# Performance work log

Hardware: AMD Instinct MI355X
Metric: run time of the kernel (lower is better)

The kernel has to match this reference:

```python
import jax, jax.numpy as jnp
import numpy as np

EPS = 1e-5

def setup_inputs() -> dict:
    key = jax.random.key(0)
    ks = jax.random.split(key, 8)
    B, T, D, S = 8, 4096, 1024, 64
    return {
        "x": jax.random.normal(ks[0], (B, T, D), dtype=jnp.float32),
        "time_decay": jax.random.normal(ks[1], (S,), dtype=jnp.float32) * 0.1 - 0.5,
        "time_first": jax.random.normal(ks[2], (S,), dtype=jnp.float32) * 0.1,
        "W_key": jax.random.normal(ks[3], (S, D), dtype=jnp.float32) * 0.02,
        "W_value": jax.random.normal(ks[4], (S, D), dtype=jnp.float32) * 0.02,
        "W_output": jax.random.normal(ks[5], (D, S), dtype=jnp.float32) * 0.02,
        "W_shift": jax.random.normal(ks[6], (D, D), dtype=jnp.float32) * 0.02,
        "shift_gate": jnp.ones((D,), dtype=jnp.float32),
        "ln_w": jnp.ones((D,), dtype=jnp.float32),
        "ln_b": jnp.zeros((D,), dtype=jnp.float32),
    }


def _forward(x, time_decay, time_first, W_key, W_value, W_output, W_shift, shift_gate, ln_w, ln_b):
    B, T, D = x.shape
    S = time_decay.shape[0]
    # --- token shift: rotate sequence by shift_len, project, gated blend ---
    shift_len = max(1, int(T * 0.5))
    x_cat = jnp.concatenate([x[:, shift_len:], x[:, :-shift_len]], axis=1)  # (B,T,D)
    gate = jax.nn.sigmoid(shift_gate)
    x_shift = jnp.einsum('btd,ed->bte', x_cat, W_shift) * gate + x * (1.0 - gate)
    # --- layernorm (torch: biased variance, eps=1e-5) ---
    mu = jnp.mean(x_shift, axis=-1, keepdims=True)
    var = jnp.mean(jnp.square(x_shift - mu), axis=-1, keepdims=True)
    xn = (x_shift - mu) * jax.lax.rsqrt(var + EPS) * ln_w + ln_b
    # --- key/value projections and per-step wkv (fully vectorized) ---
    k = jnp.einsum('btd,sd->bts', xn, W_key)    # (B,T,S)
    v = jnp.einsum('btd,sd->bts', xn, W_value)  # (B,T,S)
    wkv = jnp.exp(-jnp.exp(time_first) * jax.nn.sigmoid(k)) * v  # (B,T,S)
    # --- linear recurrence: state = state*w + wkv_t, scanned over T ---
    w = jnp.exp(time_decay)  # (S,)
    def step(state, wkv_t):
        state = state * w + wkv_t
        return state, state
    init = jnp.zeros((B, S), dtype=x.dtype)
    last_state, states = jax.lax.scan(step, init, jnp.swapaxes(wkv, 0, 1))  # states: (T,B,S)
    states = jnp.swapaxes(states, 0, 1)  # (B,T,S)
    # --- batched output projection (applied per-step in torch; same math) ---
    output = jnp.einsum('bts,ds->btd', states, W_output)  # (B,T,D)
    return output, last_state


def reference(x, time_decay, time_first, W_key, W_value, W_output, W_shift, shift_gate, ln_w, ln_b):
    out, last_state = _forward(x, time_decay, time_first, W_key, W_value, W_output, W_shift, shift_gate, ln_w, ln_b)
    return out, jax.lax.stop_gradient(last_state)
```

## Files before the change

kernel.cpp:

```cpp
#include <hip/hip_runtime.h>
#include <stdint.h>

#define B_ 8
#define T_ 4096
#define D_ 1024
#define S_ 64
#define N_ 32768
#define OUT_ELEMS 33554432
#define NCHK 128
#define CHKL 32

typedef __attribute__((ext_vector_type(8))) short bf16x8;
typedef __attribute__((ext_vector_type(8))) unsigned short u16x8;
typedef __attribute__((ext_vector_type(4))) float f32x4;

__device__ __forceinline__ uint16_t f2bf(float f) {
    union { float f; uint32_t u; } v; v.f = f;
    uint32_t r = v.u + 0x7FFFu + ((v.u >> 16) & 1u);
    return (uint16_t)(r >> 16);
}
__device__ __forceinline__ float bf2f(uint16_t h) {
    union { uint32_t u; float f; } v; v.u = ((uint32_t)h) << 16;
    return v.f;
}

#define GLOAD_LDS16(gp, lp)                                             \
    __builtin_amdgcn_global_load_lds(                                   \
        (const __attribute__((address_space(1))) void*)(gp),            \
        (__attribute__((address_space(3))) void*)(lp), 16, 0, 0)

__global__ void prep(const float* __restrict__ x,
                     const float* __restrict__ Wsf, const float* __restrict__ Wkf,
                     const float* __restrict__ Wvf, const float* __restrict__ Wof,
                     const float* __restrict__ sg, const float* __restrict__ tf,
                     const float* __restrict__ lnw, const float* __restrict__ lnb,
                     uint16_t* __restrict__ xb, uint16_t* __restrict__ Wsb,
                     uint16_t* __restrict__ Wkvb, uint16_t* __restrict__ Wob,
                     float* __restrict__ gbuf, float* __restrict__ efirst,
                     float* __restrict__ ucvec)
{
    __shared__ float red[4];
    const int blk = blockIdx.x, tid = threadIdx.x;
    if (blk < 2048) {
        for (int i = blk * 256 + tid; i < OUT_ELEMS / 4; i += 2048 * 256) {
            float4 v = ((const float4*)x)[i];
            ushort4 o;
            o.x = f2bf(v.x); o.y = f2bf(v.y); o.z = f2bf(v.z); o.w = f2bf(v.w);
            ((ushort4*)xb)[i] = o;
        }
        return;
    }
    if (blk < 3298) {
        int i = (blk - 2048) * 256 + tid;
        const float* src; uint16_t* dst; int j; bool fold = false;
        if (i < 262144) { src = Wsf; dst = Wsb; j = i; }
        else if (i < 278528) { src = Wkf; dst = Wkvb; j = i - 262144; fold = true; }
        else if (i < 294912) { src = Wvf; dst = Wkvb + 65536; j = i - 278528; fold = true; }
        else if (i < 311296) { src = Wof; dst = Wob; j = i - 294912; }
        else if (i < 311552) {
            j = i - 311296;
            float4 v = ((const float4*)sg)[j];
            float4 g;
            g.x = 1.f / (1.f + __expf(-v.x)); g.y = 1.f / (1.f + __expf(-v.y));
            g.z = 1.f / (1.f + __expf(-v.z)); g.w = 1.f / (1.f + __expf(-v.w));
            ((float4*)gbuf)[j] = g;
            return;
        } else if (i < 311568) {
            j = i - 311552;
            float4 v = ((const float4*)tf)[j];
            float4 e;
            e.x = __expf(v.x); e.y = __expf(v.y); e.z = __expf(v.z); e.w = __expf(v.w);
            ((float4*)efirst)[j] = e;
            return;
        } else return;
        float4 v = ((const float4*)src)[j];
        if (fold) {
            float4 l = ((const float4*)lnw)[j & 255];
            v.x *= l.x; v.y *= l.y; v.z *= l.z; v.w *= l.w;
        }
        ushort4 o;
        o.x = f2bf(v.x); o.y = f2bf(v.y); o.z = f2bf(v.z); o.w = f2bf(v.w);
        ((ushort4*)dst)[j] = o;
        return;
    }
    {
        int b2 = blk - 3298;
        int which = b2 >> 6, s = b2 & 63;
        const float* W = (which < 2) ? Wkf : Wvf;
        const float* L = (which & 1) ? lnb : lnw;
        float4 wv = ((const float4*)W)[s * 256 + tid];
        float4 lv = ((const float4*)L)[tid];
        float p = wv.x * lv.x + wv.y * lv.y + wv.z * lv.z + wv.w * lv.w;
#pragma unroll
        for (int off = 32; off; off >>= 1) p += __shfl_xor(p, off);
        if ((tid & 63) == 0) red[tid >> 6] = p;
        __syncthreads();
        if (tid == 0) ucvec[which * 64 + s] = red[0] + red[1] + red[2] + red[3];
    }
}

__global__ __launch_bounds__(256) void k1_shift_gemm(
    const uint16_t* __restrict__ xb, const uint16_t* __restrict__ Wsb,
    const float* __restrict__ gbuf, uint16_t* __restrict__ xs)
{
    __shared__ char sh[34816];
    uint16_t (*As)[64] = (uint16_t(*)[64])sh;
    uint16_t (*Bs)[64] = (uint16_t(*)[64])(sh + 16384);
    float (*epi)[68] = (float(*)[68])sh;

    const int tid = threadIdx.x;
    const int w = tid >> 6, lane = tid & 63, quad = lane >> 4, l16 = lane & 15;
    const int wm = w >> 1, wn = w & 1;
    const int lin = blockIdx.x;
    const int mt = (lin & 7) * 32 + (lin >> 6);
    const int nt = (lin >> 3) & 7;
    const int m0 = mt * 128, n0 = nt * 128;
    const int m0x = m0 ^ 2048;

    const int srow = w * 32 + (lane >> 3);
    const int scg  = ((lane & 7) ^ ((lane >> 3) & 7)) * 8;
    const uint16_t* aG = xb  + (size_t)(m0x + srow) * D_ + scg;
    const uint16_t* bG = Wsb + (size_t)(n0  + srow) * D_ + scg;

    f32x4 acc[4][4];
#pragma unroll
    for (int i = 0; i < 4; ++i)
#pragma unroll
        for (int j = 0; j < 4; ++j) acc[i][j] = (f32x4){0.f, 0.f, 0.f, 0.f};

    for (int k0 = 0; k0 < D_; k0 += 64) {
        __syncthreads();
#pragma unroll
        for (int i = 0; i < 4; ++i) {
            GLOAD_LDS16(aG + k0 + (size_t)(i * 8) * D_, &As[w * 32 + i * 8][0]);
            GLOAD_LDS16(bG + k0 + (size_t)(i * 8) * D_, &Bs[w * 32 + i * 8][0]);
        }
        __syncthreads();
#pragma unroll
        for (int ks = 0; ks < 2; ++ks) {
            bf16x8 a[4], b[4];
#pragma unroll
            for (int i = 0; i < 4; ++i)
                a[i] = *(const bf16x8*)&As[wm * 64 + i * 16 + l16]
                                         [(((ks * 4 + quad) ^ (l16 & 7)) * 8)];
#pragma unroll
            for (int j = 0; j < 4; ++j)
                b[j] = *(const bf16x8*)&Bs[wn * 64 + j * 16 + l16]
                                         [(((ks * 4 + quad) ^ (l16 & 7)) * 8)];
#pragma unroll
            for (int i = 0; i < 4; ++i)
#pragma unroll
                for (int j = 0; j < 4; ++j)
                    acc[i][j] = __builtin_amdgcn_mfma_f32_16x16x32_bf16(
                        a[i], b[j], acc[i][j], 0, 0, 0);
        }
    }

    const int row = tid >> 1;
    const int c0 = (tid & 1) * 32;
#pragma unroll
    for (int h = 0; h < 2; ++h) {
        __syncthreads();
        if (wn == h) {
#pragma unroll
            for (int i = 0; i < 4; ++i)
#pragma unroll
                for (int j = 0; j < 4; ++j)
#pragma unroll
                    for (int r = 0; r < 4; ++r)
                        epi[wm * 64 + i * 16 + quad * 4 + r][j * 16 + l16] =
                            acc[i][j][r];
        }
        __syncthreads();
        const int col = n0 + h * 64 + c0;
        const uint16_t* xrow = xb + (size_t)(m0 + row) * D_ + col;
        uint16_t* orow = xs + (size_t)(m0 + row) * D_ + col;
#pragma unroll
        for (int c4 = 0; c4 < 8; ++c4) {
            float4 g4 = ((const float4*)(gbuf + col))[c4];
            ushort4 xh = ((const ushort4*)xrow)[c4];
            const float* e = &epi[row][c0 + c4 * 4];
            ushort4 o;
            o.x = f2bf(e[0] * g4.x + bf2f(xh.x) * (1.f - g4.x));
            o.y = f2bf(e[1] * g4.y + bf2f(xh.y) * (1.f - g4.y));
            o.z = f2bf(e[2] * g4.z + bf2f(xh.z) * (1.f - g4.z));
            o.w = f2bf(e[3] * g4.w + bf2f(xh.w) * (1.f - g4.w));
            ((ushort4*)orow)[c4] = o;
        }
    }
}

__global__ __launch_bounds__(256) void k3_kv(
    const uint16_t* __restrict__ xsb, const uint16_t* __restrict__ Wkvb,
    const float* __restrict__ efirst, const float* __restrict__ ucvec,
    float* __restrict__ wkv)
{
    __shared__ char sh[34816];
    uint16_t (*As)[64] = (uint16_t(*)[64])sh;
    uint16_t (*Bs)[64] = (uint16_t(*)[64])(sh + 8192);
    float (*epi)[132] = (float(*)[132])sh;
    float* ssh = (float*)(sh + 33792);
    float* qsh = (float*)(sh + 34048);

    const int tid = threadIdx.x;
    const int w = tid >> 6, lane = tid & 63, quad = lane >> 4, l16 = lane & 15;
    const int wm = w >> 1, wn = w & 1;
    const int m0 = blockIdx.x * 64;

    const int lrow = w * 8 + (lane >> 3);
    const int scg  = ((lane & 7) ^ ((lane >> 3) & 7)) * 8;
    const uint16_t* aG = xsb + (size_t)(m0 + lrow) * D_ + scg;
    const uint16_t* bG = Wkvb + (size_t)lrow * D_ + scg;

    f32x4 acc[2][4];
#pragma unroll
    for (int i = 0; i < 2; ++i)
#pragma unroll
        for (int j = 0; j < 4; ++j) acc[i][j] = (f32x4){0.f, 0.f, 0.f, 0.f};
    f32x4 accs[2], accq[2];
#pragma unroll
    for (int i = 0; i < 2; ++i) {
        accs[i] = (f32x4){0.f, 0.f, 0.f, 0.f};
        accq[i] = (f32x4){0.f, 0.f, 0.f, 0.f};
    }
    bf16x8 ones;
#pragma unroll
    for (int j = 0; j < 8; ++j) ones[j] = (short)0x3F80;

    for (int k0 = 0; k0 < D_; k0 += 64) {
        __syncthreads();
#pragma unroll
        for (int i = 0; i < 2; ++i)
            GLOAD_LDS16(aG + k0 + (size_t)(i * 32) * D_, &As[w * 8 + i * 32][0]);
#pragma unroll
        for (int i = 0; i < 4; ++i)
            GLOAD_LDS16(bG + k0 + (size_t)(i * 32) * D_, &Bs[w * 8 + i * 32][0]);
        __syncthreads();
#pragma unroll
        for (int ks = 0; ks < 2; ++ks) {
            bf16x8 a[2], b[4];
#pragma unroll
            for (int i = 0; i < 2; ++i)
                a[i] = *(const bf16x8*)&As[wm * 32 + i * 16 + l16]
                                         [(((ks * 4 + quad) ^ (l16 & 7)) * 8)];
#pragma unroll
            for (int j = 0; j < 4; ++j)
                b[j] = *(const bf16x8*)&Bs[wn * 64 + j * 16 + l16]
                                         [(((ks * 4 + quad) ^ (l16 & 7)) * 8)];
#pragma unroll
            for (int i = 0; i < 2; ++i)
#pragma unroll
                for (int j = 0; j < 4; ++j)
                    acc[i][j] = __builtin_amdgcn_mfma_f32_16x16x32_bf16(
                        a[i], b[j], acc[i][j], 0, 0, 0);
            if (wn == 0) {
#pragma unroll
                for (int i = 0; i < 2; ++i) {
                    accs[i] = __builtin_amdgcn_mfma_f32_16x16x32_bf16(
                        a[i], ones, accs[i], 0, 0, 0);
                    accq[i] = __builtin_amdgcn_mfma_f32_16x16x32_bf16(
                        a[i], a[i], accq[i], 0, 0, 0);
                }
            }
        }
    }

    if (wn == 0) {
#pragma unroll
        for (int i = 0; i < 2; ++i) {
            if (l16 == 0) {
#pragma unroll
                for (int r = 0; r < 4; ++r)
                    ssh[wm * 32 + i * 16 + quad * 4 + r] = accs[i][r];
            }
            if ((l16 >> 2) == quad)
                qsh[wm * 32 + i * 16 + l16] = accq[i][l16 & 3];
        }
    }

    __syncthreads();
#pragma unroll
    for (int i = 0; i < 2; ++i)
#pragma unroll
        for (int j = 0; j < 4; ++j)
#pragma unroll
            for (int r = 0; r < 4; ++r)
                epi[wm * 32 + i * 16 + quad * 4 + r][wn * 64 + j * 16 + l16] =
                    acc[i][j][r];
    __syncthreads();

    const int row = tid >> 2, s0 = (tid & 3) * 16;
    const float mu = ssh[row] * (1.f / (float)D_);
    const float var = qsh[row] * (1.f / (float)D_) - mu * mu;
    const float rstd = rsqrtf(var + 1e-5f);
    float* dst = wkv + (size_t)(m0 + row) * S_ + s0;
#pragma unroll
    for (int c4 = 0; c4 < 4; ++c4) {
        float4 kk = *(const float4*)&epi[row][s0 + c4 * 4];
        float4 vv = *(const float4*)&epi[row][64 + s0 + c4 * 4];
        float4 uk4 = *(const float4*)(ucvec + 0 * 64 + s0 + c4 * 4);
        float4 ck4 = *(const float4*)(ucvec + 1 * 64 + s0 + c4 * 4);
        float4 uv4 = *(const float4*)(ucvec + 2 * 64 + s0 + c4 * 4);
        float4 cv4 = *(const float4*)(ucvec + 3 * 64 + s0 + c4 * 4);
        float4 ef = ((const float4*)(efirst + s0))[c4];
        float kx = rstd * (kk.x - mu * uk4.x) + ck4.x;
        float ky = rstd * (kk.y - mu * uk4.y) + ck4.y;
        float kz = rstd * (kk.z - mu * uk4.z) + ck4.z;
        float kw = rstd * (kk.w - mu * uk4.w) + ck4.w;
        float vx = rstd * (vv.x - mu * uv4.x) + cv4.x;
        float vy = rstd * (vv.y - mu * uv4.y) + cv4.y;
        float vz = rstd * (vv.z - mu * uv4.z) + cv4.z;
        float vw = rstd * (vv.w - mu * uv4.w) + cv4.w;
        float4 o;
        o.x = __expf(-ef.x / (1.f + __expf(-kx))) * vx;
        o.y = __expf(-ef.y / (1.f + __expf(-ky))) * vy;
        o.z = __expf(-ef.z / (1.f + __expf(-kz))) * vz;
        o.w = __expf(-ef.w / (1.f + __expf(-kw))) * vw;
        *(float4*)(dst + c4 * 4) = o;
    }
}

__global__ void k4a(const float* __restrict__ wkv,
                    const float* __restrict__ time_decay,
                    float* __restrict__ part)
{
    const int s = threadIdx.x;
    const int bc = blockIdx.x;
    const int b = bc >> 7, c = bc & (NCHK - 1);
    float w = expf(time_decay[s]);
    const float* src = wkv + ((size_t)b * T_ + c * CHKL) * S_ + s;
    float st = 0.f;
#pragma unroll
    for (int t = 0; t < CHKL; ++t) st = st * w + src[(size_t)t * S_];
    part[(size_t)bc * S_ + s] = st;
}
__global__ void k4bc(const float* __restrict__ wkv,
                     const float* __restrict__ time_decay,
                     const float* __restrict__ part,
                     uint16_t* __restrict__ stb,
                     float* __restrict__ last_state)
{
    const int s = threadIdx.x;
    const int bc = blockIdx.x;
    const int b = bc >> 7, c = bc & (NCHK - 1);
    const float td = time_decay[s];
    const float w = expf(td);
    const float wL = expf(td * (float)CHKL);
    const float* pp = part + (size_t)b * NCHK * S_ + s;
    float cin = 0.f;
#pragma unroll 4
    for (int j = 0; j < c; ++j) cin = cin * wL + pp[(size_t)j * S_];
    const float* src = wkv + ((size_t)b * T_ + c * CHKL) * S_ + s;
    uint16_t* dst = stb + ((size_t)b * T_ + c * CHKL) * S_ + s;
    float st = cin;
#pragma unroll
    for (int t = 0; t < CHKL; ++t) {
        st = st * w + src[(size_t)t * S_];
        dst[(size_t)t * S_] = f2bf(st);
    }
    if (c == NCHK - 1) last_state[b * S_ + s] = st;
}

__global__ __launch_bounds__(256) void k5_out(
    const uint16_t* __restrict__ st, const uint16_t* __restrict__ Wob,
    float* __restrict__ out)
{
    __shared__ float epi[128][68];
    const int tid = threadIdx.x;
    const int w = tid >> 6, lane = tid & 63, quad = lane >> 4, l16 = lane & 15;
    const int wm = w >> 1, wn = w & 1;
    const int m0b = blockIdx.y * 128;
    const int n0b = blockIdx.x * 128;

    f32x4 acc[4][4];
#pragma unroll
    for (int i = 0; i < 4; ++i)
#pragma unroll
        for (int j = 0; j < 4; ++j) acc[i][j] = (f32x4){0.f, 0.f, 0.f, 0.f};

#pragma unroll
    for (int k = 0; k < S_; k += 32) {
        bf16x8 a[4], b[4];
#pragma unroll
        for (int i = 0; i < 4; ++i)
            a[i] = *(const bf16x8*)(st + (size_t)(m0b + wm * 64 + i * 16 + l16) * S_ + k + quad * 8);
#pragma unroll
        for (int i = 0; i < 4; ++i)
            b[i] = *(const bf16x8*)(Wob + (size_t)(n0b + wn * 64 + i * 16 + l16) * S_ + k + quad * 8);
#pragma unroll
        for (int i = 0; i < 4; ++i)
#pragma unroll
            for (int j = 0; j < 4; ++j)
                acc[i][j] = __builtin_amdgcn_mfma_f32_16x16x32_bf16(
                    a[i], b[j], acc[i][j], 0, 0, 0);
    }

    const int row = tid >> 1;
    const int c0 = (tid & 1) * 32;
#pragma unroll
    for (int h = 0; h < 2; ++h) {
        __syncthreads();
        if (wn == h) {
#pragma unroll
            for (int i = 0; i < 4; ++i)
#pragma unroll
                for (int j = 0; j < 4; ++j)
#pragma unroll
                    for (int r = 0; r < 4; ++r)
                        epi[wm * 64 + i * 16 + quad * 4 + r][j * 16 + l16] =
                            acc[i][j][r];
        }
        __syncthreads();
        float* dst = out + (size_t)(m0b + row) * D_ + n0b + h * 64 + c0;
#pragma unroll
        for (int c4 = 0; c4 < 8; ++c4)
            ((float4*)dst)[c4] = *(const float4*)&epi[row][c0 + c4 * 4];
    }
}

extern "C" void kernel_launch(void* const* d_in, const int* in_sizes, int n_in,
                              void* d_out, int out_size, void* d_ws, size_t ws_size,
                              hipStream_t stream) {
    const float* x          = (const float*)d_in[0];
    const float* time_decay = (const float*)d_in[1];
    const float* time_first = (const float*)d_in[2];
    const float* W_key      = (const float*)d_in[3];
    const float* W_value    = (const float*)d_in[4];
    const float* W_output   = (const float*)d_in[5];
    const float* W_shift    = (const float*)d_in[6];
    const float* shift_gate = (const float*)d_in[7];
    const float* ln_w       = (const float*)d_in[8];
    const float* ln_b       = (const float*)d_in[9];
    float* out = (float*)d_out;

    char* ws = (char*)d_ws;
    uint16_t* xb      = (uint16_t*)(ws + 0);
    uint16_t* xs      = (uint16_t*)(ws + 67108864);
    float*    wkv     = (float*)   (ws + 134217728);
    uint16_t* stb     = (uint16_t*)(ws + 142606336);
    uint16_t* Wsb     = (uint16_t*)(ws + 146800640);
    uint16_t* Wkvb    = (uint16_t*)(ws + 148897792);
    uint16_t* Wob     = (uint16_t*)(ws + 149159936);
    float*    part    = (float*)   (ws + 149291008);
    float*    gbuf    = (float*)   (ws + 149815296);
    float*    efirst  = (float*)   (ws + 149819392);
    float*    ucvec   = (float*)   (ws + 149819648);

    prep<<<3554, 256, 0, stream>>>(x, W_shift, W_key, W_value, W_output,
                                   shift_gate, time_first, ln_w, ln_b,
                                   xb, Wsb, Wkvb, Wob, gbuf, efirst, ucvec);
    k1_shift_gemm<<<2048, 256, 0, stream>>>(xb, Wsb, gbuf, xs);
    k3_kv<<<512, 256, 0, stream>>>(xs, Wkvb, efirst, ucvec, wkv);
    k4a<<<B_ * NCHK, S_, 0, stream>>>(wkv, time_decay, part);
    k4bc<<<B_ * NCHK, S_, 0, stream>>>(wkv, time_decay, part, stb, out + OUT_ELEMS);
    k5_out<<<dim3(8, 256), 256, 0, stream>>>(stb, Wob, out);
}
```

Baseline: 436.4 us.

## Triple-buffer shift GEMM with 256x128 tiles and async LDS prefetch

Rewrites the token-shift GEMM kernel to use 512-thread blocks computing 256x128 tiles. A three-slot LDS ring lets global-to-LDS loads for step k+2 be issued in pieces between the MFMA phases of step k, with explicit vmcnt waits and barriers replacing the load-sync-compute-sync loop. MFMA bursts are wrapped in s_setprio. The epilogue is reorganised for the larger tile. The aim is to hide memory latency and raise MFMA utilisation. In exchange, the 144KB of LDS limits occupancy to one block per CU, and the hand-counted waitcnt scheme is fragile.

```diff
diff --git a/kernel.cpp b/kernel.cpp
--- a/kernel.cpp
+++ b/kernel.cpp
@@ -99,28 +99,36 @@
     }
 }
 
-__global__ __launch_bounds__(256) void k1_shift_gemm(
+__global__ __launch_bounds__(512, 2) void k1_shift_gemm(
     const uint16_t* __restrict__ xb, const uint16_t* __restrict__ Wsb,
     const float* __restrict__ gbuf, uint16_t* __restrict__ xs)
 {
-    __shared__ char sh[34816];
-    uint16_t (*As)[64] = (uint16_t(*)[64])sh;
-    uint16_t (*Bs)[64] = (uint16_t(*)[64])(sh + 16384);
-    float (*epi)[68] = (float(*)[68])sh;
+    __shared__ char sh[147456];
+    char* const slot0 = sh;
+    char* const slot1 = sh + 49152;
+    char* const slot2 = sh + 98304;
 
     const int tid = threadIdx.x;
     const int w = tid >> 6, lane = tid & 63, quad = lane >> 4, l16 = lane & 15;
     const int wm = w >> 1, wn = w & 1;
+    const int w8 = w * 8;
+
     const int lin = blockIdx.x;
-    const int mt = (lin & 7) * 32 + (lin >> 6);
-    const int nt = (lin >> 3) & 7;
-    const int m0 = mt * 128, n0 = nt * 128;
+    const int idx = lin >> 3;
+    const int nt = idx & 7;
+    const int mt = (lin & 7) * 16 + (idx >> 3);
+    const int m0 = mt * 256, n0 = nt * 128;
     const int m0x = m0 ^ 2048;
 
-    const int srow = w * 32 + (lane >> 3);
+    const int arow = w8 + (lane >> 3);
     const int scg  = ((lane & 7) ^ ((lane >> 3) & 7)) * 8;
-    const uint16_t* aG = xb  + (size_t)(m0x + srow) * D_ + scg;
-    const uint16_t* bG = Wsb + (size_t)(n0  + srow) * D_ + scg;
+    const uint16_t* aBase = xb  + (size_t)(m0x + arow) * D_ + scg;
+    const uint16_t* bBase = Wsb + (size_t)(n0  + arow) * D_ + scg;
+
+    const int swz0 = ((quad) ^ (l16 & 7)) * 8;
+    const int swz1 = ((4 + quad) ^ (l16 & 7)) * 8;
+    const int aRow = wm * 64 + l16;
+    const int bRow = wn * 64 + l16;
 
     f32x4 acc[4][4];
 #pragma unroll
@@ -128,58 +136,114 @@
 #pragma unroll
         for (int j = 0; j < 4; ++j) acc[i][j] = (f32x4){0.f, 0.f, 0.f, 0.f};
 
-    for (int k0 = 0; k0 < D_; k0 += 64) {
-        __syncthreads();
-#pragma unroll
-        for (int i = 0; i < 4; ++i) {
-            GLOAD_LDS16(aG + k0 + (size_t)(i * 8) * D_, &As[w * 32 + i * 8][0]);
-            GLOAD_LDS16(bG + k0 + (size_t)(i * 8) * D_, &Bs[w * 32 + i * 8][0]);
-        }
-        __syncthreads();
-#pragma unroll
-        for (int ks = 0; ks < 2; ++ks) {
-            bf16x8 a[4], b[4];
-#pragma unroll
-            for (int i = 0; i < 4; ++i)
-                a[i] = *(const bf16x8*)&As[wm * 64 + i * 16 + l16]
-                                         [(((ks * 4 + quad) ^ (l16 & 7)) * 8)];
-#pragma unroll
-            for (int j = 0; j < 4; ++j)
-                b[j] = *(const bf16x8*)&Bs[wn * 64 + j * 16 + l16]
-                                         [(((ks * 4 + quad) ^ (l16 & 7)) * 8)];
-#pragma unroll
-            for (int i = 0; i < 4; ++i)
-#pragma unroll
-                for (int j = 0; j < 4; ++j)
-                    acc[i][j] = __builtin_amdgcn_mfma_f32_16x16x32_bf16(
-                        a[i], b[j], acc[i][j], 0, 0, 0);
-        }
-    }
-
-    const int row = tid >> 1;
-    const int c0 = (tid & 1) * 32;
-#pragma unroll
-    for (int h = 0; h < 2; ++h) {
-        __syncthreads();
-        if (wn == h) {
-#pragma unroll
-            for (int i = 0; i < 4; ++i)
-#pragma unroll
-                for (int j = 0; j < 4; ++j)
+    {
+        uint16_t (*A0)[64] = (uint16_t(*)[64])slot0;
+        uint16_t (*B0)[64] = (uint16_t(*)[64])(slot0 + 32768);
+        uint16_t (*A1)[64] = (uint16_t(*)[64])slot1;
+        uint16_t (*B1)[64] = (uint16_t(*)[64])(slot1 + 32768);
+#pragma unroll
+        for (int c = 0; c < 4; ++c)
+            GLOAD_LDS16(aBase + (size_t)(c * 64) * D_ + 0, &A0[c * 64 + w8][0]);
+#pragma unroll
+        for (int c = 0; c < 2; ++c)
+            GLOAD_LDS16(bBase + (size_t)(c * 64) * D_ + 0, &B0[c * 64 + w8][0]);
+#pragma unroll
+        for (int c = 0; c < 4; ++c)
+            GLOAD_LDS16(aBase + (size_t)(c * 64) * D_ + 64, &A1[c * 64 + w8][0]);
+#pragma unroll
+        for (int c = 0; c < 2; ++c)
+            GLOAD_LDS16(bBase + (size_t)(c * 64) * D_ + 64, &B1[c * 64 + w8][0]);
+    }
+    asm volatile("s_waitcnt vmcnt(6)" ::: "memory");
+    __builtin_amdgcn_s_barrier();
+
+    int ci = 0;
+#pragma unroll 1
+    for (int t = 0; t < 16; ++t) {
+        char* scur = (ci == 0) ? slot0 : (ci == 1) ? slot1 : slot2;
+        const int ci2 = (ci + 2 >= 3) ? ci - 1 : ci + 2;
+        char* s2 = (ci2 == 0) ? slot0 : (ci2 == 1) ? slot1 : slot2;
+        uint16_t (*Ac)[64] = (uint16_t(*)[64])scur;
+        uint16_t (*Bc)[64] = (uint16_t(*)[64])(scur + 32768);
+        uint16_t (*A2)[64] = (uint16_t(*)[64])s2;
+        uint16_t (*B2)[64] = (uint16_t(*)[64])(s2 + 32768);
+        const int kb2 = (t + 2) * 64;
+
+#pragma unroll
+        for (int p = 0; p < 4; ++p) {
+            const int mh = p >> 1, nh = p & 1;
+            bf16x8 av[2][2], bv[2][2];
+#pragma unroll
+            for (int q = 0; q < 2; ++q) {
+                av[q][0] = *(const bf16x8*)&Ac[aRow + (mh * 2 + q) * 16][swz0];
+                av[q][1] = *(const bf16x8*)&Ac[aRow + (mh * 2 + q) * 16][swz1];
+                bv[q][0] = *(const bf16x8*)&Bc[bRow + (nh * 2 + q) * 16][swz0];
+                bv[q][1] = *(const bf16x8*)&Bc[bRow + (nh * 2 + q) * 16][swz1];
+            }
+            if (t < 14) {
+                if (p == 0) {
+                    GLOAD_LDS16(aBase + (size_t)(0 * 64) * D_ + kb2, &A2[0 * 64 + w8][0]);
+                    GLOAD_LDS16(aBase + (size_t)(1 * 64) * D_ + kb2, &A2[1 * 64 + w8][0]);
+                } else if (p == 1) {
+                    GLOAD_LDS16(aBase + (size_t)(2 * 64) * D_ + kb2, &A2[2 * 64 + w8][0]);
+                    GLOAD_LDS16(aBase + (size_t)(3 * 64) * D_ + kb2, &A2[3 * 64 + w8][0]);
+                } else if (p == 2) {
+                    GLOAD_LDS16(bBase + (size_t)(0 * 64) * D_ + kb2, &B2[0 * 64 + w8][0]);
+                } else {
+                    GLOAD_LDS16(bBase + (size_t)(1 * 64) * D_ + kb2, &B2[1 * 64 + w8][0]);
+                }
+            }
+            if (p == 3) {
+                if (t < 14) {
+                    asm volatile("s_waitcnt vmcnt(6)" ::: "memory");
+                } else if (t == 14) {
+                    asm volatile("s_waitcnt vmcnt(0)" ::: "memory");
+                }
+            }
+            __builtin_amdgcn_s_barrier();
+            __builtin_amdgcn_s_setprio(1);
+#pragma unroll
+            for (int q = 0; q < 2; ++q)
+#pragma unroll
+                for (int r = 0; r < 2; ++r) {
+                    acc[mh * 2 + q][nh * 2 + r] =
+                        __builtin_amdgcn_mfma_f32_16x16x32_bf16(
+                            av[q][0], bv[r][0], acc[mh * 2 + q][nh * 2 + r], 0, 0, 0);
+                    acc[mh * 2 + q][nh * 2 + r] =
+                        __builtin_amdgcn_mfma_f32_16x16x32_bf16(
+                            av[q][1], bv[r][1], acc[mh * 2 + q][nh * 2 + r], 0, 0, 0);
+                }
+            __builtin_amdgcn_s_setprio(0);
+            __builtin_amdgcn_s_barrier();
+        }
+        ci = (ci + 1 >= 3) ? 0 : ci + 1;
+    }
+
+    float (*epi)[132] = (float(*)[132])sh;
+    const int row = tid >> 3;
+    const int cb = (tid & 7) * 16;
+#pragma unroll
+    for (int mb = 0; mb < 4; ++mb) {
+        __syncthreads();
+        if (wm == mb) {
+#pragma unroll
+            for (int mi = 0; mi < 4; ++mi)
+#pragma unroll
+                for (int ni = 0; ni < 4; ++ni)
 #pragma unroll
                     for (int r = 0; r < 4; ++r)
-                        epi[wm * 64 + i * 16 + quad * 4 + r][j * 16 + l16] =
-                            acc[i][j][r];
-        }
-        __syncthreads();
-        const int col = n0 + h * 64 + c0;
-        const uint16_t* xrow = xb + (size_t)(m0 + row) * D_ + col;
-        uint16_t* orow = xs + (size_t)(m0 + row) * D_ + col;
-#pragma unroll
-        for (int c4 = 0; c4 < 8; ++c4) {
-            float4 g4 = ((const float4*)(gbuf + col))[c4];
+                        epi[mi * 16 + quad * 4 + r][wn * 64 + ni * 16 + l16] =
+                            acc[mi][ni][r];
+        }
+        __syncthreads();
+        const int grow = m0 + mb * 64 + row;
+        const uint16_t* xrow = xb + (size_t)grow * D_ + n0 + cb;
+        uint16_t* orow = xs + (size_t)grow * D_ + n0 + cb;
+#pragma unroll
+        for (int c4 = 0; c4 < 4; ++c4) {
+            float4 g4 = ((const float4*)(gbuf + n0 + cb))[c4];
             ushort4 xh = ((const ushort4*)xrow)[c4];
-            const float* e = &epi[row][c0 + c4 * 4];
+            const float* e = &epi[row][cb + c4 * 4];
             ushort4 o;
             o.x = f2bf(e[0] * g4.x + bf2f(xh.x) * (1.f - g4.x));
             o.y = f2bf(e[1] * g4.y + bf2f(xh.y) * (1.f - g4.y));
@@ -449,7 +513,7 @@
     prep<<<3554, 256, 0, stream>>>(x, W_shift, W_key, W_value, W_output,
                                    shift_gate, time_first, ln_w, ln_b,
                                    xb, Wsb, Wkvb, Wob, gbuf, efirst, ucvec);
-    k1_shift_gemm<<<2048, 256, 0, stream>>>(xb, Wsb, gbuf, xs);
+    k1_shift_gemm<<<1024, 512, 0, stream>>>(xb, Wsb, gbuf, xs);
     k3_kv<<<512, 256, 0, stream>>>(xs, Wkvb, efirst, ucvec, wkv);
     k4a<<<B_ * NCHK, S_, 0, stream>>>(wkv, time_decay, part);
     k4bc<<<B_ * NCHK, S_, 0, stream>>>(wkv, time_decay, part, stb, out + OUT_ELEMS);
```

Result: no change. 442.0 us (+1.3%).

## Enlarge shift GEMM tiles to 256x256 with double-buffered LDS prefetch

Applied to the files above, without the earlier changes.

Rewrites the token-shift GEMM to use 256x256 output tiles over 512 threads (8 waves, 128x64 per wave), launching 512 blocks instead of 2048. Global-to-LDS loads for the next K slice are issued into a second LDS buffer while MFMAs run on the current one. Wave priority is raised around the MFMA bursts. This aims to raise arithmetic intensity and hide load latency, at the cost of 128KB LDS per block and more accumulator registers, which limits occupancy.

```diff
diff --git a/kernel.cpp b/kernel.cpp
--- a/kernel.cpp
+++ b/kernel.cpp
@@ -99,85 +99,118 @@
     }
 }
 
-__global__ __launch_bounds__(256) void k1_shift_gemm(
+__global__ __launch_bounds__(512, 2) void k1_shift_gemm(
     const uint16_t* __restrict__ xb, const uint16_t* __restrict__ Wsb,
     const float* __restrict__ gbuf, uint16_t* __restrict__ xs)
 {
-    __shared__ char sh[34816];
-    uint16_t (*As)[64] = (uint16_t(*)[64])sh;
-    uint16_t (*Bs)[64] = (uint16_t(*)[64])(sh + 16384);
-    float (*epi)[68] = (float(*)[68])sh;
+    __shared__ char sh[131072];
 
     const int tid = threadIdx.x;
     const int w = tid >> 6, lane = tid & 63, quad = lane >> 4, l16 = lane & 15;
-    const int wm = w >> 1, wn = w & 1;
+    const int wm = w >> 2, wn = w & 3;
+    const int w8 = w * 8;
+
     const int lin = blockIdx.x;
-    const int mt = (lin & 7) * 32 + (lin >> 6);
-    const int nt = (lin >> 3) & 7;
-    const int m0 = mt * 128, n0 = nt * 128;
+    const int idx = lin >> 3;
+    const int nt = idx & 3;
+    const int mt = (lin & 7) * 16 + (idx >> 2);
+    const int m0 = mt * 256, n0 = nt * 256;
     const int m0x = m0 ^ 2048;
 
-    const int srow = w * 32 + (lane >> 3);
+    const int arow = w8 + (lane >> 3);
     const int scg  = ((lane & 7) ^ ((lane >> 3) & 7)) * 8;
-    const uint16_t* aG = xb  + (size_t)(m0x + srow) * D_ + scg;
-    const uint16_t* bG = Wsb + (size_t)(n0  + srow) * D_ + scg;
-
-    f32x4 acc[4][4];
-#pragma unroll
-    for (int i = 0; i < 4; ++i)
+    const uint16_t* aBase = xb  + (size_t)(m0x + arow) * D_ + scg;
+    const uint16_t* bBase = Wsb + (size_t)(n0  + arow) * D_ + scg;
+
+    const int swz0 = ((quad) ^ (l16 & 7)) * 8;
+    const int swz1 = ((4 + quad) ^ (l16 & 7)) * 8;
+    const int aRowBase = wm * 128 + l16;
+    const int bRowBase = wn * 64 + l16;
+
+    f32x4 acc[8][4];
+#pragma unroll
+    for (int i = 0; i < 8; ++i)
 #pragma unroll
         for (int j = 0; j < 4; ++j) acc[i][j] = (f32x4){0.f, 0.f, 0.f, 0.f};
 
-    for (int k0 = 0; k0 < D_; k0 += 64) {
-        __syncthreads();
-#pragma unroll
-        for (int i = 0; i < 4; ++i) {
-            GLOAD_LDS16(aG + k0 + (size_t)(i * 8) * D_, &As[w * 32 + i * 8][0]);
-            GLOAD_LDS16(bG + k0 + (size_t)(i * 8) * D_, &Bs[w * 32 + i * 8][0]);
-        }
-        __syncthreads();
+    {
+        uint16_t (*A0)[64] = (uint16_t(*)[64])(sh);
+        uint16_t (*B0)[64] = (uint16_t(*)[64])(sh + 32768);
+#pragma unroll
+        for (int c = 0; c < 4; ++c) {
+            GLOAD_LDS16(aBase + (size_t)(c * 64) * D_, &A0[c * 64 + w8][0]);
+            GLOAD_LDS16(bBase + (size_t)(c * 64) * D_, &B0[c * 64 + w8][0]);
+        }
+    }
+    asm volatile("s_waitcnt vmcnt(0)" ::: "memory");
+    __builtin_amdgcn_s_barrier();
+
+#pragma unroll 1
+    for (int t = 0; t < 16; ++t) {
+        const int c = t & 1, o = c ^ 1;
+        uint16_t (*Ac)[64] = (uint16_t(*)[64])(sh + c * 65536);
+        uint16_t (*Bc)[64] = (uint16_t(*)[64])(sh + c * 65536 + 32768);
+        uint16_t (*Ao)[64] = (uint16_t(*)[64])(sh + o * 65536);
+        uint16_t (*Bo)[64] = (uint16_t(*)[64])(sh + o * 65536 + 32768);
+        const int kb1 = (t + 1) * 64;
+
 #pragma unroll
         for (int ks = 0; ks < 2; ++ks) {
-            bf16x8 a[4], b[4];
-#pragma unroll
-            for (int i = 0; i < 4; ++i)
-                a[i] = *(const bf16x8*)&As[wm * 64 + i * 16 + l16]
-                                         [(((ks * 4 + quad) ^ (l16 & 7)) * 8)];
-#pragma unroll
-            for (int j = 0; j < 4; ++j)
-                b[j] = *(const bf16x8*)&Bs[wn * 64 + j * 16 + l16]
-                                         [(((ks * 4 + quad) ^ (l16 & 7)) * 8)];
-#pragma unroll
-            for (int i = 0; i < 4; ++i)
-#pragma unroll
-                for (int j = 0; j < 4; ++j)
-                    acc[i][j] = __builtin_amdgcn_mfma_f32_16x16x32_bf16(
-                        a[i], b[j], acc[i][j], 0, 0, 0);
-        }
-    }
-
-    const int row = tid >> 1;
-    const int c0 = (tid & 1) * 32;
-#pragma unroll
-    for (int h = 0; h < 2; ++h) {
-        __syncthreads();
-        if (wn == h) {
-#pragma unroll
-            for (int i = 0; i < 4; ++i)
-#pragma unroll
-                for (int j = 0; j < 4; ++j)
+            const int swz = ks ? swz1 : swz0;
+            bf16x8 a[8], b[4];
+#pragma unroll
+            for (int mf = 0; mf < 8; ++mf)
+                a[mf] = *(const bf16x8*)&Ac[aRowBase + mf * 16][swz];
+#pragma unroll
+            for (int nf = 0; nf < 4; ++nf)
+                b[nf] = *(const bf16x8*)&Bc[bRowBase + nf * 16][swz];
+            if (ks == 0 && t < 15) {
+#pragma unroll
+                for (int cc = 0; cc < 4; ++cc) {
+                    GLOAD_LDS16(aBase + (size_t)(cc * 64) * D_ + kb1,
+                                &Ao[cc * 64 + w8][0]);
+                    GLOAD_LDS16(bBase + (size_t)(cc * 64) * D_ + kb1,
+                                &Bo[cc * 64 + w8][0]);
+                }
+            }
+            if (ks == 1 && t < 15) {
+                asm volatile("s_waitcnt vmcnt(0)" ::: "memory");
+            }
+            __builtin_amdgcn_s_barrier();
+            __builtin_amdgcn_s_setprio(1);
+#pragma unroll
+            for (int mf = 0; mf < 8; ++mf)
+#pragma unroll
+                for (int nf = 0; nf < 4; ++nf)
+                    acc[mf][nf] = __builtin_amdgcn_mfma_f32_16x16x32_bf16(
+                        a[mf], b[nf], acc[mf][nf], 0, 0, 0);
+            __builtin_amdgcn_s_setprio(0);
+        }
+    }
+
+    float (*epi)[260] = (float(*)[260])sh;
+    const int row = tid >> 3;
+    const int c0 = (tid & 7) * 32;
+#pragma unroll
+    for (int mb = 0; mb < 4; ++mb) {
+        __syncthreads();
+        if (wm == (mb >> 1)) {
+#pragma unroll
+            for (int mf = 0; mf < 4; ++mf)
+#pragma unroll
+                for (int nf = 0; nf < 4; ++nf)
 #pragma unroll
                     for (int r = 0; r < 4; ++r)
-                        epi[wm * 64 + i * 16 + quad * 4 + r][j * 16 + l16] =
-                            acc[i][j][r];
-        }
-        __syncthreads();
-        const int col = n0 + h * 64 + c0;
-        const uint16_t* xrow = xb + (size_t)(m0 + row) * D_ + col;
-        uint16_t* orow = xs + (size_t)(m0 + row) * D_ + col;
+                        epi[mf * 16 + quad * 4 + r][wn * 64 + nf * 16 + l16] =
+                            acc[(mb & 1) * 4 + mf][nf][r];
+        }
+        __syncthreads();
+        const int grow = m0 + mb * 64 + row;
+        const uint16_t* xrow = xb + (size_t)grow * D_ + n0 + c0;
+        uint16_t* orow = xs + (size_t)grow * D_ + n0 + c0;
 #pragma unroll
         for (int c4 = 0; c4 < 8; ++c4) {
-            float4 g4 = ((const float4*)(gbuf + col))[c4];
+            float4 g4 = ((const float4*)(gbuf + n0 + c0))[c4];
             ushort4 xh = ((const ushort4*)xrow)[c4];
             const float* e = &epi[row][c0 + c4 * 4];
             ushort4 o;
@@ -449,7 +482,7 @@
     prep<<<3554, 256, 0, stream>>>(x, W_shift, W_key, W_value, W_output,
                                    shift_gate, time_first, ln_w, ln_b,
                                    xb, Wsb, Wkvb, Wob, gbuf, efirst, ucvec);
-    k1_shift_gemm<<<2048, 256, 0, stream>>>(xb, Wsb, gbuf, xs);
+    k1_shift_gemm<<<512, 512, 0, stream>>>(xb, Wsb, gbuf, xs);
     k3_kv<<<512, 256, 0, stream>>>(xs, Wkvb, efirst, ucvec, wkv);
     k4a<<<B_ * NCHK, S_, 0, stream>>>(wkv, time_decay, part);
     k4bc<<<B_ * NCHK, S_, 0, stream>>>(wkv, time_decay, part, stb, out + OUT_ELEMS);
```

Result: faster. 426.7 us (-2.2%).
